# Performance work log

Hardware: AMD Instinct MI355X
Metric: run time of the kernel (lower is better)

## Reference

```python
import jax, jax.numpy as jnp
import numpy as np

B, S, E, H = 2, 2048, 1024, 16
HD = E // H


def setup_inputs() -> dict:
    key = jax.random.key(0)
    ks = jax.random.split(key, 5)
    scale = 1.0 / np.sqrt(E)
    return {
        "query": jax.random.normal(ks[0], (B, S, E), jnp.float32),
        "key": jax.random.normal(ks[1], (B, S, E), jnp.float32),
        "value": jax.random.normal(ks[2], (B, S, E), jnp.float32),
        "qkv_w": jax.random.normal(ks[3], (3 * E, E), jnp.float32) * scale,
        "qkv_b": jnp.zeros((3 * E,), jnp.float32),
        "out_w": jax.random.normal(ks[4], (E, E), jnp.float32) * scale,
        "out_b": jnp.zeros((E,), jnp.float32),
    }


def reference(query, key, value, qkv_w, qkv_b, out_w, out_b):
    # Fused QKV projection from query (module ignores key/value contents)
    qkv = query @ qkv_w.T + qkv_b                      # [B,S,3E]
    qkv = qkv.reshape(B, S, 3, H, HD)
    q = qkv[:, :, 0].transpose(0, 2, 1, 3)             # [B,H,S,HD]
    k = qkv[:, :, 1].transpose(0, 2, 1, 3)
    v = qkv[:, :, 2].transpose(0, 2, 1, 3)
    scaling = 1.0 / np.sqrt(HD)
    scores = jnp.einsum("bhqd,bhkd->bhqk", q, k) * scaling  # [B,H,S,S]
    probs = jax.nn.softmax(scores, axis=-1)
    ctx = jnp.einsum("bhqk,bhkd->bhqd", probs, v)      # [B,H,S,HD]
    ctx = ctx.transpose(0, 2, 1, 3).reshape(B, S, E)
    return ctx @ out_w.T + out_b
```

## Files before the change

### kernel.cpp

```cpp
#include <hip/hip_runtime.h>
#include <hip/hip_bf16.h>
#include <math.h>

#define BB 2
#define SS 2048
#define EE 1024
#define HH 16
#define HD 64

typedef __bf16 bf16;
typedef __bf16 bf16x8 __attribute__((ext_vector_type(8)));
typedef float floatx4 __attribute__((ext_vector_type(4)));
typedef float floatx16 __attribute__((ext_vector_type(16)));

#define MFMA(a, b, c) __builtin_amdgcn_mfma_f32_16x16x32_bf16(a, b, c, 0, 0, 0)
#define MFMA32(a, b, c) __builtin_amdgcn_mfma_f32_32x32x16_bf16(a, b, c, 0, 0, 0)

__device__ inline void async16(const bf16* g, bf16* l) {
    __builtin_amdgcn_global_load_lds(
        (const __attribute__((address_space(1))) void*)g,
        (__attribute__((address_space(3))) void*)l, 16, 0, 0);
}

__device__ inline unsigned cvt_pk_bf16(float a, float b) {
    unsigned r;
    asm("v_cvt_pk_bf16_f32 %0, %1, %2" : "=v"(r) : "v"(a), "v"(b));
    return r;
}

__global__ __launch_bounds__(256) void cvt3(
    const float* __restrict__ a, const float* __restrict__ b,
    const float* __restrict__ c,
    bf16* __restrict__ oa, bf16* __restrict__ ob, bf16* __restrict__ oc) {
    const long NA = (long)4096 * 1024, NB = (long)3072 * 1024, NC = (long)1024 * 1024;
    const long total = (NA + NB + NC) >> 2;
    long i = (long)blockIdx.x * blockDim.x + threadIdx.x;
    const long stride = (long)gridDim.x * blockDim.x;
    for (; i < total; i += stride) {
        const long e = i << 2;
        const float* src;
        bf16* dst;
        if (e < NA)           { src = a + e;            dst = oa + e; }
        else if (e < NA + NB) { src = b + (e - NA);     dst = ob + (e - NA); }
        else                  { src = c + (e - NA - NB); dst = oc + (e - NA - NB); }
        float4 v = *(const float4*)src;
        union { bf16 h[4]; uint2 u; } t;
        t.h[0] = (bf16)v.x; t.h[1] = (bf16)v.y; t.h[2] = (bf16)v.z; t.h[3] = (bf16)v.w;
        *(uint2*)dst = t.u;
    }
}

__global__ __launch_bounds__(256) void qkv_gemm(
    const bf16* __restrict__ A, const bf16* __restrict__ W,
    const float* __restrict__ bias,
    bf16* __restrict__ Qw, bf16* __restrict__ Kw, bf16* __restrict__ Vtw) {
    __shared__ __align__(16) bf16 As[2][128 * 64];
    __shared__ __align__(16) bf16 Bs[2][128 * 64];
    const int tid  = threadIdx.x;
    const int wave = tid >> 6, lane = tid & 63;
    const int quad = lane >> 4, l16 = lane & 15;
    const int wr = wave >> 1, wc = wave & 1;
    const int m0 = blockIdx.y * 128, n0 = blockIdx.x * 128;
    const int lr = lane >> 3;
    const int lcs = ((lane & 7) ^ (lr & 7)) * 8;
    const int rsw = (l16 & 7) << 3;

    const bf16* Ag = A + (long)(m0 + wave * 32 + lr) * 1024 + lcs;
    const bf16* Bg = W + (long)(n0 + wave * 32 + lr) * 1024 + lcs;
    const int lbase = (wave * 32) * 64 + lane * 8;

    floatx4 acc[4][4] = {};

#pragma unroll
    for (int j = 0; j < 4; ++j) {
        async16(Ag + (long)j * 8 * 1024, &As[0][lbase + j * 8 * 64]);
        async16(Bg + (long)j * 8 * 1024, &Bs[0][lbase + j * 8 * 64]);
    }

    for (int ks = 0; ks < 16; ++ks) {
        __syncthreads();
        const int cur = ks & 1;
        if (ks < 15) {
            const int nxt = cur ^ 1, k0 = (ks + 1) * 64;
#pragma unroll
            for (int j = 0; j < 4; ++j) {
                async16(Ag + (long)j * 8 * 1024 + k0, &As[nxt][lbase + j * 8 * 64]);
                async16(Bg + (long)j * 8 * 1024 + k0, &Bs[nxt][lbase + j * 8 * 64]);
            }
        }
#pragma unroll
        for (int c = 0; c < 2; ++c) {
            bf16x8 af[4], bfr[4];
#pragma unroll
            for (int mi = 0; mi < 4; ++mi)
                af[mi] = *(const bf16x8*)&As[cur][(wr * 64 + mi * 16 + l16) * 64 + ((c * 32 + quad * 8) ^ rsw)];
#pragma unroll
            for (int ni = 0; ni < 4; ++ni)
                bfr[ni] = *(const bf16x8*)&Bs[cur][(wc * 64 + ni * 16 + l16) * 64 + ((c * 32 + quad * 8) ^ rsw)];
#pragma unroll
            for (int mi = 0; mi < 4; ++mi)
#pragma unroll
                for (int ni = 0; ni < 4; ++ni)
                    acc[mi][ni] = MFMA(af[mi], bfr[ni], acc[mi][ni]);
        }
    }

#pragma unroll
    for (int mi = 0; mi < 4; ++mi)
#pragma unroll
        for (int ni = 0; ni < 4; ++ni) {
            const int n = n0 + wc * 64 + ni * 16 + l16;
            const float bn = bias[n];
            const int sel = n >> 10;
            const int e = n & 1023, h = e >> 6, d = e & 63;
            if (sel == 2) {
                const int m_base = m0 + wr * 64 + mi * 16 + quad * 4;
                const int b = m_base >> 11, s0 = m_base & 2047;
                union { bf16 h4[4]; uint2 u; } t;
#pragma unroll
                for (int r = 0; r < 4; ++r)
                    t.h4[r] = (bf16)(acc[mi][ni][r] + bn);
                *(uint2*)&Vtw[((long)(b * HH + h) * HD + d) * SS + s0] = t.u;
            } else {
#pragma unroll
                for (int r = 0; r < 4; ++r) {
                    const int m = m0 + wr * 64 + mi * 16 + quad * 4 + r;
                    const int b = m >> 11, s = m & 2047;
                    const float v = acc[mi][ni][r] + bn;
                    if (sel == 0)
                        Qw[((long)(b * HH + h) * SS + s) * HD + d] = (bf16)(v * 0.125f);
                    else
                        Kw[((long)(b * HH + h) * SS + s) * HD + d] = (bf16)v;
                }
            }
        }
}

__global__ __launch_bounds__(256) void attn(
    const bf16* __restrict__ Qw, const bf16* __restrict__ Kw,
    const bf16* __restrict__ Vtw, bf16* __restrict__ ctxw) {
    __shared__ __align__(16) bf16 Kt[64 * 64];
    __shared__ __align__(16) bf16 Vt[64 * 64];

    const int tid = threadIdx.x;
    const int wave = tid >> 6, lane = tid & 63;
    const int l5 = lane & 31, hi = lane >> 5;
    const int qb = blockIdx.x, bh = blockIdx.y;
    const bf16* Qh = Qw  + (long)bh * SS * HD;
    const bf16* Kh = Kw  + (long)bh * SS * HD;
    const bf16* Vh = Vtw + (long)bh * HD * SS;

    const int qbase = qb * 128 + wave * 32;
    bf16x8 qf[4];
#pragma unroll
    for (int d0 = 0; d0 < 4; ++d0)
        qf[d0] = *(const bf16x8*)&Qh[(long)(qbase + l5) * HD + d0 * 16 + hi * 8];

    floatx16 ctx0 = {}, ctx1 = {};
    float lsum = 0.f;

    const int srow = tid >> 2;
    const int sc0  = (tid & 3) * 16;
    const int swz  = (srow & 7) << 3;
    const int rswz = (l5 & 7) << 3;
    bf16* Kl0 = &Kt[srow * 64 + (sc0 ^ swz)];
    bf16* Kl1 = &Kt[srow * 64 + ((sc0 + 8) ^ swz)];
    bf16* Vl0 = &Vt[srow * 64 + (sc0 ^ swz)];
    bf16* Vl1 = &Vt[srow * 64 + ((sc0 + 8) ^ swz)];

    uint4 kr0, kr1, vr0, vr1;
    {
        const uint4* ks = (const uint4*)&Kh[(long)srow * HD + sc0];
        kr0 = ks[0]; kr1 = ks[1];
        const uint4* vs = (const uint4*)&Vh[(long)srow * SS + sc0];
        vr0 = vs[0]; vr1 = vs[1];
    }

    for (int kt = 0; kt < 32; ++kt) {
        __syncthreads();
        *(uint4*)Kl0 = kr0;
        *(uint4*)Kl1 = kr1;
        *(uint4*)Vl0 = vr0;
        *(uint4*)Vl1 = vr1;
        __syncthreads();

        if (kt < 31) {
            const uint4* ks = (const uint4*)&Kh[(long)((kt + 1) * 64 + srow) * HD + sc0];
            kr0 = ks[0]; kr1 = ks[1];
            const uint4* vs = (const uint4*)&Vh[(long)srow * SS + (kt + 1) * 64 + sc0];
            vr0 = vs[0]; vr1 = vs[1];
        }

        floatx16 sf[2];
#pragma unroll
        for (int kb = 0; kb < 2; ++kb) {
            floatx16 s = {};
#pragma unroll
            for (int d0 = 0; d0 < 4; ++d0) {
                const bf16x8 af = *(const bf16x8*)
                    &Kt[(kb * 32 + l5) * 64 + ((d0 * 16 + hi * 8) ^ rswz)];
                s = MFMA32(af, qf[d0], s);
            }
            sf[kb] = s;
        }

#pragma unroll
        for (int kb = 0; kb < 2; ++kb) {
#pragma unroll
            for (int r = 0; r < 16; ++r) {
                const float p = __expf(sf[kb][r]);
                sf[kb][r] = p;
                lsum += p;
            }
            unsigned w[8];
#pragma unroll
            for (int i = 0; i < 8; ++i)
                w[i] = cvt_pk_bf16(sf[kb][2 * i], sf[kb][2 * i + 1]);
            asm("v_permlane32_swap_b32 %0, %1" : "+v"(w[0]), "+v"(w[2]));
            asm("v_permlane32_swap_b32 %0, %1" : "+v"(w[1]), "+v"(w[3]));
            asm("v_permlane32_swap_b32 %0, %1" : "+v"(w[4]), "+v"(w[6]));
            asm("v_permlane32_swap_b32 %0, %1" : "+v"(w[5]), "+v"(w[7]));
            union { unsigned u[4]; bf16x8 v; } pa0 = {{w[0], w[1], w[2], w[3]}},
                                               pa1 = {{w[4], w[5], w[6], w[7]}};
#pragma unroll
            for (int kc = 0; kc < 2; ++kc) {
                const bf16x8 pa = kc ? pa1.v : pa0.v;
                const int kcol = kb * 32 + kc * 16 + hi * 8;
                const bf16x8 vf0 = *(const bf16x8*)&Vt[l5 * 64 + (kcol ^ rswz)];
                const bf16x8 vf1 = *(const bf16x8*)&Vt[(32 + l5) * 64 + (kcol ^ rswz)];
                ctx0 = MFMA32(pa, vf0, ctx0);
                ctx1 = MFMA32(pa, vf1, ctx1);
            }
        }
    }

    const float rs  = lsum + __shfl_xor(lsum, 32, 64);
    const float inv = 1.0f / rs;

    const int b = bh >> 4, h = bh & 15;
#pragma unroll
    for (int r = 0; r < 16; ++r) {
        const int qrow = (r & 3) + 8 * (r >> 2) + 4 * hi;
        const float iq = __shfl(inv, qrow, 64);
        const long base = ((long)b * SS + qbase + qrow) * EE + h * HD;
        ctxw[base + l5]      = (bf16)(ctx0[r] * iq);
        ctxw[base + 32 + l5] = (bf16)(ctx1[r] * iq);
    }
}

__global__ __launch_bounds__(256) void out_gemm(
    const bf16* __restrict__ A, const bf16* __restrict__ W,
    const float* __restrict__ bias, float* __restrict__ out) {
    __shared__ __align__(16) bf16 As[2][64 * 64];
    __shared__ __align__(16) bf16 Bs[2][128 * 64];
    const int tid  = threadIdx.x;
    const int wave = tid >> 6, lane = tid & 63;
    const int quad = lane >> 4, l16 = lane & 15;
    const int wr = wave & 1, wc = wave >> 1;
    const int m0 = blockIdx.y * 64, n0 = blockIdx.x * 128;
    const int lr = lane >> 3;
    const int lcs = ((lane & 7) ^ (lr & 7)) * 8;
    const int rsw = (l16 & 7) << 3;

    const bf16* Ag = A + (long)(m0 + wave * 16 + lr) * 1024 + lcs;
    const bf16* Bg = W + (long)(n0 + wave * 32 + lr) * 1024 + lcs;
    const int labase = (wave * 16) * 64 + lane * 8;
    const int lbbase = (wave * 32) * 64 + lane * 8;

    floatx4 acc[2][4] = {};

#pragma unroll
    for (int j = 0; j < 2; ++j)
        async16(Ag + (long)j * 8 * 1024, &As[0][labase + j * 8 * 64]);
#pragma unroll
    for (int j = 0; j < 4; ++j)
        async16(Bg + (long)j * 8 * 1024, &Bs[0][lbbase + j * 8 * 64]);

    for (int ks = 0; ks < 16; ++ks) {
        __syncthreads();
        const int cur = ks & 1;
        if (ks < 15) {
            const int nxt = cur ^ 1, k0 = (ks + 1) * 64;
#pragma unroll
            for (int j = 0; j < 2; ++j)
                async16(Ag + (long)j * 8 * 1024 + k0, &As[nxt][labase + j * 8 * 64]);
#pragma unroll
            for (int j = 0; j < 4; ++j)
                async16(Bg + (long)j * 8 * 1024 + k0, &Bs[nxt][lbbase + j * 8 * 64]);
        }
#pragma unroll
        for (int c = 0; c < 2; ++c) {
            bf16x8 af[2], bfr[4];
#pragma unroll
            for (int mi = 0; mi < 2; ++mi)
                af[mi] = *(const bf16x8*)&As[cur][(wr * 32 + mi * 16 + l16) * 64 + ((c * 32 + quad * 8) ^ rsw)];
#pragma unroll
            for (int ni = 0; ni < 4; ++ni)
                bfr[ni] = *(const bf16x8*)&Bs[cur][(wc * 64 + ni * 16 + l16) * 64 + ((c * 32 + quad * 8) ^ rsw)];
#pragma unroll
            for (int mi = 0; mi < 2; ++mi)
#pragma unroll
                for (int ni = 0; ni < 4; ++ni)
                    acc[mi][ni] = MFMA(af[mi], bfr[ni], acc[mi][ni]);
        }
    }

#pragma unroll
    for (int mi = 0; mi < 2; ++mi)
#pragma unroll
        for (int ni = 0; ni < 4; ++ni) {
            const int n = n0 + wc * 64 + ni * 16 + l16;
            const float bn = bias[n];
#pragma unroll
            for (int r = 0; r < 4; ++r) {
                const int m = m0 + wr * 32 + mi * 16 + quad * 4 + r;
                out[(long)m * 1024 + n] = acc[mi][ni][r] + bn;
            }
        }
}

extern "C" void kernel_launch(void* const* d_in, const int* in_sizes, int n_in,
                              void* d_out, int out_size, void* d_ws, size_t ws_size,
                              hipStream_t stream) {
    const float* query = (const float*)d_in[0];
    const float* qkv_w = (const float*)d_in[3];
    const float* qkv_b = (const float*)d_in[4];
    const float* out_w = (const float*)d_in[5];
    const float* out_b = (const float*)d_in[6];

    const long NTOK = (long)BB * SS;
    bf16* qb   = (bf16*)d_ws;
    bf16* wqb  = qb  + NTOK * EE;
    bf16* owb  = wqb + (long)3 * EE * EE;
    bf16* Qw   = owb + (long)EE * EE;
    bf16* Kw   = Qw  + NTOK * EE;
    bf16* Vtw  = Kw  + NTOK * EE;
    bf16* ctxw = qb;
    float* out = (float*)d_out;

    cvt3<<<2048, 256, 0, stream>>>(query, qkv_w, out_w, qb, wqb, owb);
    qkv_gemm<<<dim3(24, 32), 256, 0, stream>>>(qb, wqb, qkv_b, Qw, Kw, Vtw);
    attn<<<dim3(16, 32), 256, 0, stream>>>(Qw, Kw, Vtw, ctxw);
    out_gemm<<<dim3(8, 64), 256, 0, stream>>>(ctxw, owb, out_b, out);
}
```

Measured before the change: 219.1 us.

## Double-buffer attention K/V tiles with async global-to-LDS loads and exp2 softmax

Replaces the register-staged K/V tile copy with global_load_lds async loads into double-buffered shared memory, prefetching the next tile while the current one is computed and dropping one barrier per iteration. It folds log2(e) into the Q scaling so softmax can use the raw v_exp_f32 instruction instead of __expf. It also raises wave priority around the MFMA sections. The risks are double the LDS footprint and a possible race: no explicit wait on the async loads is visible before the tile is read, so correctness depends on the barrier also covering the async load counter.

Measured after the change: 217.0 us. About the same (-0.9%).

```diff
diff --git a/kernel.cpp b/kernel.cpp
--- a/kernel.cpp
+++ b/kernel.cpp
@@ -25,6 +25,12 @@
 __device__ inline unsigned cvt_pk_bf16(float a, float b) {
     unsigned r;
     asm("v_cvt_pk_bf16_f32 %0, %1, %2" : "=v"(r) : "v"(a), "v"(b));
+    return r;
+}
+
+__device__ inline float fast_exp2(float x) {
+    float r;
+    asm("v_exp_f32 %0, %1" : "=v"(r) : "v"(x));
     return r;
 }
 
@@ -128,7 +134,7 @@
                     const int b = m >> 11, s = m & 2047;
                     const float v = acc[mi][ni][r] + bn;
                     if (sel == 0)
-                        Qw[((long)(b * HH + h) * SS + s) * HD + d] = (bf16)(v * 0.125f);
+                        Qw[((long)(b * HH + h) * SS + s) * HD + d] = (bf16)(v * 0.18033688f);
                     else
                         Kw[((long)(b * HH + h) * SS + s) * HD + d] = (bf16)v;
                 }
@@ -139,8 +145,8 @@
 __global__ __launch_bounds__(256) void attn(
     const bf16* __restrict__ Qw, const bf16* __restrict__ Kw,
     const bf16* __restrict__ Vtw, bf16* __restrict__ ctxw) {
-    __shared__ __align__(16) bf16 Kt[64 * 64];
-    __shared__ __align__(16) bf16 Vt[64 * 64];
+    __shared__ __align__(16) bf16 Kts[2][64 * 64];
+    __shared__ __align__(16) bf16 Vts[2][64 * 64];
 
     const int tid = threadIdx.x;
     const int wave = tid >> 6, lane = tid & 63;
@@ -159,48 +165,46 @@
     floatx16 ctx0 = {}, ctx1 = {};
     float lsum = 0.f;
 
-    const int srow = tid >> 2;
-    const int sc0  = (tid & 3) * 16;
-    const int swz  = (srow & 7) << 3;
+    const int wrow = wave * 8 + (lane >> 3);
+    const int sch  = ((lane & 7) ^ ((lane >> 3) & 7)) * 8;
+    const bf16* Kg0 = Kh + (long)wrow * HD + sch;
+    const bf16* Kg1 = Kh + (long)(32 + wrow) * HD + sch;
+    const bf16* Vg0 = Vh + (long)wrow * SS + sch;
+    const bf16* Vg1 = Vh + (long)(32 + wrow) * SS + sch;
+    const int ldst = wave * 512 + lane * 8;
     const int rswz = (l5 & 7) << 3;
-    bf16* Kl0 = &Kt[srow * 64 + (sc0 ^ swz)];
-    bf16* Kl1 = &Kt[srow * 64 + ((sc0 + 8) ^ swz)];
-    bf16* Vl0 = &Vt[srow * 64 + (sc0 ^ swz)];
-    bf16* Vl1 = &Vt[srow * 64 + ((sc0 + 8) ^ swz)];
-
-    uint4 kr0, kr1, vr0, vr1;
-    {
-        const uint4* ks = (const uint4*)&Kh[(long)srow * HD + sc0];
-        kr0 = ks[0]; kr1 = ks[1];
-        const uint4* vs = (const uint4*)&Vh[(long)srow * SS + sc0];
-        vr0 = vs[0]; vr1 = vs[1];
-    }
+
+    async16(Kg0, &Kts[0][ldst]);
+    async16(Kg1, &Kts[0][ldst + 2048]);
+    async16(Vg0, &Vts[0][ldst]);
+    async16(Vg1, &Vts[0][ldst + 2048]);
 
     for (int kt = 0; kt < 32; ++kt) {
         __syncthreads();
-        *(uint4*)Kl0 = kr0;
-        *(uint4*)Kl1 = kr1;
-        *(uint4*)Vl0 = vr0;
-        *(uint4*)Vl1 = vr1;
-        __syncthreads();
 
         if (kt < 31) {
-            const uint4* ks = (const uint4*)&Kh[(long)((kt + 1) * 64 + srow) * HD + sc0];
-            kr0 = ks[0]; kr1 = ks[1];
-            const uint4* vs = (const uint4*)&Vh[(long)srow * SS + (kt + 1) * 64 + sc0];
-            vr0 = vs[0]; vr1 = vs[1];
-        }
+            const int nb = (kt + 1) & 1;
+            const long ko = (long)(kt + 1) * 64;
+            async16(Kg0 + ko * HD, &Kts[nb][ldst]);
+            async16(Kg1 + ko * HD, &Kts[nb][ldst + 2048]);
+            async16(Vg0 + ko,      &Vts[nb][ldst]);
+            async16(Vg1 + ko,      &Vts[nb][ldst + 2048]);
+        }
+        const bf16* Kc = Kts[kt & 1];
+        const bf16* Vc = Vts[kt & 1];
 
         floatx16 sf[2];
 #pragma unroll
         for (int kb = 0; kb < 2; ++kb) {
             floatx16 s = {};
+            __builtin_amdgcn_s_setprio(1);
 #pragma unroll
             for (int d0 = 0; d0 < 4; ++d0) {
                 const bf16x8 af = *(const bf16x8*)
-                    &Kt[(kb * 32 + l5) * 64 + ((d0 * 16 + hi * 8) ^ rswz)];
+                    &Kc[(kb * 32 + l5) * 64 + ((d0 * 16 + hi * 8) ^ rswz)];
                 s = MFMA32(af, qf[d0], s);
             }
+            __builtin_amdgcn_s_setprio(0);
             sf[kb] = s;
         }
 
@@ -208,7 +212,7 @@
         for (int kb = 0; kb < 2; ++kb) {
 #pragma unroll
             for (int r = 0; r < 16; ++r) {
-                const float p = __expf(sf[kb][r]);
+                const float p = fast_exp2(sf[kb][r]);
                 sf[kb][r] = p;
                 lsum += p;
             }
@@ -226,10 +230,12 @@
             for (int kc = 0; kc < 2; ++kc) {
                 const bf16x8 pa = kc ? pa1.v : pa0.v;
                 const int kcol = kb * 32 + kc * 16 + hi * 8;
-                const bf16x8 vf0 = *(const bf16x8*)&Vt[l5 * 64 + (kcol ^ rswz)];
-                const bf16x8 vf1 = *(const bf16x8*)&Vt[(32 + l5) * 64 + (kcol ^ rswz)];
+                const bf16x8 vf0 = *(const bf16x8*)&Vc[l5 * 64 + (kcol ^ rswz)];
+                const bf16x8 vf1 = *(const bf16x8*)&Vc[(32 + l5) * 64 + (kcol ^ rswz)];
+                __builtin_amdgcn_s_setprio(1);
                 ctx0 = MFMA32(pa, vf0, ctx0);
                 ctx1 = MFMA32(pa, vf1, ctx1);
+                __builtin_amdgcn_s_setprio(0);
             }
         }
     }
```
